# Kernel optimization log

Hardware: AMD Instinct MI355X
Metric: run time of the kernel (lower is better)

Reference implementation:

```python
import jax, jax.numpy as jnp
import numpy as np

SINKHORN_ITERS = 20
EPS = 1e-6


def sinkhorn(M, n_iter=SINKHORN_ITERS, eps=EPS):
    # Project (n, n) logits onto the Birkhoff polytope (doubly stochastic).
    A = jnp.exp(M - jnp.max(M, axis=(-2, -1), keepdims=True))
    for _ in range(n_iter):
        A = A / (A.sum(axis=-1, keepdims=True) + eps)
        A = A / (A.sum(axis=-2, keepdims=True) + eps)
    return A


def setup_inputs() -> dict:
    key = jax.random.key(0)
    k1, k2, k3, k4 = jax.random.split(key, 4)
    B, S, D, E = 4, 4096, 4096, 4
    return {
        "x": jax.random.normal(k1, (B, S, D), dtype=jnp.float32),
        "H_res_logits": jax.random.normal(k2, (E, E), dtype=jnp.float32),
        "H_pre_logits": jax.random.normal(k3, (E, D), dtype=jnp.float32),
        "H_post_logits": jax.random.normal(k4, (E, D), dtype=jnp.float32),
    }


def reference(x, H_res_logits, H_pre_logits, H_post_logits):
    # MHCLayer forward with layer=None (residual routing only), sinkhorn projection.
    H_res = sinkhorn(H_res_logits)                      # (E, E) doubly stochastic
    H_pre = jax.nn.softmax(H_pre_logits, axis=-1)       # (E, D)
    H_post = jax.nn.softmax(H_post_logits, axis=-1)     # (E, D)

    # x_pre = (x.unsqueeze(-2) * H_pre).sum(-1)  ==  x @ H_pre^T
    x_pre = jnp.einsum("bsd,ed->bse", x, H_pre)         # (B, S, E)
    out_exp = x_pre @ H_res                             # (B, S, E)
    # out = (out_exp.unsqueeze(-1) * H_post).sum(-2)  ==  out_exp @ H_post
    out = jnp.einsum("bse,ed->bsd", out_exp, H_post)    # (B, S, D)
    return out
```

## Files before the change

kernel.cpp:

```cpp
#include <hip/hip_runtime.h>
#include <math.h>

#define E 4
#define TPB 256
#define RPB 8
#define NWAVES (TPB / 64)
#define SINKHORN_ITERS 20
#define SINKHORN_EPS 1e-6f

typedef float f4 __attribute__((ext_vector_type(4)));


__global__ __launch_bounds__(TPB) void prep_stats(
    const float* __restrict__ Hres_l,
    const float* __restrict__ Hpre_l,
    const float* __restrict__ Hpost_l,
    float* __restrict__ ws_small,
    int D4)
{
    const int t = threadIdx.x;
    const int wave = t >> 6;
    const int lane = t & 63;

    if (blockIdx.x == 8) {
        if (wave == 0) {
            float a = (lane < E * E) ? Hres_l[lane] : -1e30f;
            float m = a;
#pragma unroll
            for (int off = 1; off < 16; off <<= 1)
                m = fmaxf(m, __shfl_xor(m, off, 16));
            a = expf(a - m);
            for (int it = 0; it < SINKHORN_ITERS; ++it) {
                float rs = a;
                rs += __shfl_xor(rs, 1, 4);
                rs += __shfl_xor(rs, 2, 4);
                a /= (rs + SINKHORN_EPS);
                float cs = a;
                cs += __shfl_xor(cs, 4, 16);
                cs += __shfl_xor(cs, 8, 16);
                a /= (cs + SINKHORN_EPS);
            }
            if (lane < E * E) ws_small[lane] = a;
        }
        return;
    }

    __shared__ float redm[NWAVES], reds[NWAVES];
    const int p = blockIdx.x;
    const int mat = p >> 2, e = p & 3;
    const f4* rowp = (const f4*)((mat ? Hpost_l : Hpre_l) + (size_t)e * D4 * 4);

    float m = -1e30f;
    for (int i = t; i < D4; i += TPB) {
        f4 v = rowp[i];
        m = fmaxf(fmaxf(fmaxf(m, v.x), v.y), fmaxf(v.z, v.w));
    }
#pragma unroll
    for (int off = 1; off < 64; off <<= 1)
        m = fmaxf(m, __shfl_xor(m, off, 64));
    if (lane == 0) redm[wave] = m;
    __syncthreads();
    m = fmaxf(fmaxf(redm[0], redm[1]), fmaxf(redm[2], redm[3]));

    float s = 0.f;
    for (int i = t; i < D4; i += TPB) {
        f4 v = rowp[i];
        s += expf(v.x - m) + expf(v.y - m) + expf(v.z - m) + expf(v.w - m);
    }
#pragma unroll
    for (int off = 1; off < 64; off <<= 1)
        s += __shfl_xor(s, off, 64);
    if (lane == 0) reds[wave] = s;
    __syncthreads();
    if (t == 0) {
        ws_small[16 + p] = m;
        ws_small[24 + p] = reds[0] + reds[1] + reds[2] + reds[3];
    }
}

__global__ __launch_bounds__(TPB) void prep_write(
    const float* __restrict__ Hpre_l,
    const float* __restrict__ Hpost_l,
    const float* __restrict__ ws_small,
    f4* __restrict__ wpre4,
    f4* __restrict__ wpost4,
    int D4)
{
    const int i = blockIdx.x * TPB + threadIdx.x;
    if (i >= D4) return;

    float hres[E * E];
#pragma unroll
    for (int k = 0; k < E * E; ++k) hres[k] = ws_small[k];
    float mpre[E], spre[E], mpost[E], spost[E];
#pragma unroll
    for (int e = 0; e < E; ++e) {
        mpre[e]  = ws_small[16 + e];     spre[e]  = 1.f / ws_small[24 + e];
        mpost[e] = ws_small[16 + E + e]; spost[e] = 1.f / ws_small[24 + E + e];
    }

    const f4* pre_l4  = (const f4*)Hpre_l;
    const f4* post_l4 = (const f4*)Hpost_l;
    f4 postv[E];
#pragma unroll
    for (int e = 0; e < E; ++e) {
        f4 v = pre_l4[(size_t)e * D4 + i];
        f4 o;
        o.x = expf(v.x - mpre[e]) * spre[e];
        o.y = expf(v.y - mpre[e]) * spre[e];
        o.z = expf(v.z - mpre[e]) * spre[e];
        o.w = expf(v.w - mpre[e]) * spre[e];
        wpre4[(size_t)e * D4 + i] = o;
        f4 w = post_l4[(size_t)e * D4 + i];
        postv[e].x = expf(w.x - mpost[e]) * spost[e];
        postv[e].y = expf(w.y - mpost[e]) * spost[e];
        postv[e].z = expf(w.z - mpost[e]) * spost[e];
        postv[e].w = expf(w.w - mpost[e]) * spost[e];
    }
#pragma unroll
    for (int ep = 0; ep < E; ++ep) {
        f4 o = hres[ep * E + 0] * postv[0] + hres[ep * E + 1] * postv[1] +
               hres[ep * E + 2] * postv[2] + hres[ep * E + 3] * postv[3];
        wpost4[(size_t)ep * D4 + i] = o;
    }
}

__global__ __launch_bounds__(TPB) void xpre_kernel(
    const f4* __restrict__ x4,
    const f4* __restrict__ pre4,
    float* __restrict__ xpre,
    int D4, int chunks)
{
    __shared__ float wred[NWAVES][RPB * E];
    const int t = threadIdx.x;
    const int wave = t >> 6;
    const int lane = t & 63;
    const long row0 = (long)blockIdx.x * RPB;

    float val[RPB * E];
#pragma unroll
    for (int i = 0; i < RPB * E; ++i) val[i] = 0.f;

    for (int k = 0; k < chunks; ++k) {
        const int d4 = k * TPB + t;
        f4 hp[E];
#pragma unroll
        for (int e = 0; e < E; ++e) hp[e] = pre4[(size_t)e * D4 + d4];
#pragma unroll
        for (int r = 0; r < RPB; ++r) {
            f4 xv = __builtin_nontemporal_load(&x4[(row0 + r) * D4 + d4]);
#pragma unroll
            for (int e = 0; e < E; ++e)
                val[r * E + e] += xv.x * hp[e].x + xv.y * hp[e].y +
                                  xv.z * hp[e].z + xv.w * hp[e].w;
        }
    }

    {
        const bool h0 = lane & 1;
        float a16[16];
#pragma unroll
        for (int i = 0; i < 16; ++i) {
            float send = h0 ? val[2 * i] : val[2 * i + 1];
            float recv = __shfl_xor(send, 1, 64);
            a16[i] = (h0 ? val[2 * i + 1] : val[2 * i]) + recv;
        }
        const bool h1 = (lane >> 1) & 1;
        float a8[8];
#pragma unroll
        for (int i = 0; i < 8; ++i) {
            float send = h1 ? a16[2 * i] : a16[2 * i + 1];
            float recv = __shfl_xor(send, 2, 64);
            a8[i] = (h1 ? a16[2 * i + 1] : a16[2 * i]) + recv;
        }
        const bool h2 = (lane >> 2) & 1;
        float a4[4];
#pragma unroll
        for (int i = 0; i < 4; ++i) {
            float send = h2 ? a8[2 * i] : a8[2 * i + 1];
            float recv = __shfl_xor(send, 4, 64);
            a4[i] = (h2 ? a8[2 * i + 1] : a8[2 * i]) + recv;
        }
        const bool h3 = (lane >> 3) & 1;
        float a2[2];
#pragma unroll
        for (int i = 0; i < 2; ++i) {
            float send = h3 ? a4[2 * i] : a4[2 * i + 1];
            float recv = __shfl_xor(send, 8, 64);
            a2[i] = (h3 ? a4[2 * i + 1] : a4[2 * i]) + recv;
        }
        const bool h4 = (lane >> 4) & 1;
        float send = h4 ? a2[0] : a2[1];
        float recv = __shfl_xor(send, 16, 64);
        float a1 = (h4 ? a2[1] : a2[0]) + recv;
        a1 += __shfl_xor(a1, 32, 64);
        if (lane < 32) wred[wave][lane] = a1;
    }
    __syncthreads();

    if (t < RPB * E) {
        float s = wred[0][t] + wred[1][t] + wred[2][t] + wred[3][t];
        const int r = t >> 2, e = t & 3;
        xpre[(row0 + r) * E + e] = s;
    }
}

__global__ __launch_bounds__(TPB) void out_kernel(
    const float* __restrict__ xpre,
    const f4* __restrict__ post4,
    f4* __restrict__ out4,
    int D4, int chunks)
{
    __shared__ float sxp[RPB * E];
    const int t = threadIdx.x;
    const long row0 = (long)blockIdx.x * RPB;

    if (t < RPB * E) sxp[t] = xpre[row0 * E + t];
    __syncthreads();

    float xp[RPB][E];
#pragma unroll
    for (int r = 0; r < RPB; ++r)
#pragma unroll
        for (int e = 0; e < E; ++e) xp[r][e] = sxp[r * E + e];

    for (int k = 0; k < chunks; ++k) {
        const int d4 = k * TPB + t;
        f4 hq[E];
#pragma unroll
        for (int e = 0; e < E; ++e) hq[e] = post4[(size_t)e * D4 + d4];
#pragma unroll
        for (int r = 0; r < RPB; ++r) {
            f4 o = xp[r][0] * hq[0] + xp[r][1] * hq[1] +
                   xp[r][2] * hq[2] + xp[r][3] * hq[3];
            __builtin_nontemporal_store(o, &out4[(row0 + r) * D4 + d4]);
        }
    }
}

extern "C" void kernel_launch(void* const* d_in, const int* in_sizes, int n_in,
                              void* d_out, int out_size, void* d_ws, size_t ws_size,
                              hipStream_t stream) {
    const float* x     = (const float*)d_in[0];
    const float* Hres  = (const float*)d_in[1];
    const float* Hpre  = (const float*)d_in[2];
    const float* Hpost = (const float*)d_in[3];
    float* out = (float*)d_out;

    const int D = in_sizes[2] / E;
    const long rows = (long)in_sizes[0] / D;
    const int D4 = D / 4;
    const int chunks = D4 / TPB;

    float* ws_pre   = (float*)d_ws;
    float* ws_post2 = ws_pre + (size_t)E * D;
    float* ws_small = ws_post2 + (size_t)E * D;
    float* ws_xpre  = ws_small + 32;

    prep_stats<<<9, TPB, 0, stream>>>(Hres, Hpre, Hpost, ws_small, D4);
    prep_write<<<(D4 + TPB - 1) / TPB, TPB, 0, stream>>>(
        Hpre, Hpost, ws_small, (f4*)ws_pre, (f4*)ws_post2, D4);

    const int grid = (int)(rows / RPB);
    xpre_kernel<<<grid, TPB, 0, stream>>>((const f4*)x, (const f4*)ws_pre,
                                          ws_xpre, D4, chunks);
    out_kernel<<<grid, TPB, 0, stream>>>(ws_xpre, (const f4*)ws_post2,
                                         (f4*)out, D4, chunks);
}
```

Baseline: 111.0 us.

## Merge softmax prep kernels and fold Sinkhorn into output kernel

Combines the two softmax preparation kernels into one kernel per row that computes max, sum and the normalized write, removing one launch. The Sinkhorn projection moves into every out_kernel block, and H_res is applied to the per-row x_pre values instead of being premultiplied into H_post. This removes a small-kernel launch and dependency from the critical path. In exchange, each output block repeats the 20-iteration Sinkhorn computation redundantly, and the prep kernel now runs on only 8 blocks doing three passes.

```diff
diff --git a/kernel.cpp b/kernel.cpp
--- a/kernel.cpp
+++ b/kernel.cpp
@@ -11,44 +11,21 @@
 typedef float f4 __attribute__((ext_vector_type(4)));
 
 
-__global__ __launch_bounds__(TPB) void prep_stats(
-    const float* __restrict__ Hres_l,
+__global__ __launch_bounds__(TPB) void prep(
     const float* __restrict__ Hpre_l,
     const float* __restrict__ Hpost_l,
-    float* __restrict__ ws_small,
+    f4* __restrict__ wpre4,
+    f4* __restrict__ wpost4,
     int D4)
 {
+    __shared__ float redm[NWAVES], reds[NWAVES];
     const int t = threadIdx.x;
     const int wave = t >> 6;
     const int lane = t & 63;
-
-    if (blockIdx.x == 8) {
-        if (wave == 0) {
-            float a = (lane < E * E) ? Hres_l[lane] : -1e30f;
-            float m = a;
-#pragma unroll
-            for (int off = 1; off < 16; off <<= 1)
-                m = fmaxf(m, __shfl_xor(m, off, 16));
-            a = expf(a - m);
-            for (int it = 0; it < SINKHORN_ITERS; ++it) {
-                float rs = a;
-                rs += __shfl_xor(rs, 1, 4);
-                rs += __shfl_xor(rs, 2, 4);
-                a /= (rs + SINKHORN_EPS);
-                float cs = a;
-                cs += __shfl_xor(cs, 4, 16);
-                cs += __shfl_xor(cs, 8, 16);
-                a /= (cs + SINKHORN_EPS);
-            }
-            if (lane < E * E) ws_small[lane] = a;
-        }
-        return;
-    }
-
-    __shared__ float redm[NWAVES], reds[NWAVES];
     const int p = blockIdx.x;
     const int mat = p >> 2, e = p & 3;
     const f4* rowp = (const f4*)((mat ? Hpost_l : Hpre_l) + (size_t)e * D4 * 4);
+    f4* dst = (mat ? wpost4 : wpre4) + (size_t)e * D4;
 
     float m = -1e30f;
     for (int i = t; i < D4; i += TPB) {
@@ -72,56 +49,16 @@
         s += __shfl_xor(s, off, 64);
     if (lane == 0) reds[wave] = s;
     __syncthreads();
-    if (t == 0) {
-        ws_small[16 + p] = m;
-        ws_small[24 + p] = reds[0] + reds[1] + reds[2] + reds[3];
-    }
-}
-
-__global__ __launch_bounds__(TPB) void prep_write(
-    const float* __restrict__ Hpre_l,
-    const float* __restrict__ Hpost_l,
-    const float* __restrict__ ws_small,
-    f4* __restrict__ wpre4,
-    f4* __restrict__ wpost4,
-    int D4)
-{
-    const int i = blockIdx.x * TPB + threadIdx.x;
-    if (i >= D4) return;
-
-    float hres[E * E];
-#pragma unroll
-    for (int k = 0; k < E * E; ++k) hres[k] = ws_small[k];
-    float mpre[E], spre[E], mpost[E], spost[E];
-#pragma unroll
-    for (int e = 0; e < E; ++e) {
-        mpre[e]  = ws_small[16 + e];     spre[e]  = 1.f / ws_small[24 + e];
-        mpost[e] = ws_small[16 + E + e]; spost[e] = 1.f / ws_small[24 + E + e];
-    }
-
-    const f4* pre_l4  = (const f4*)Hpre_l;
-    const f4* post_l4 = (const f4*)Hpost_l;
-    f4 postv[E];
-#pragma unroll
-    for (int e = 0; e < E; ++e) {
-        f4 v = pre_l4[(size_t)e * D4 + i];
+    const float inv = 1.f / (reds[0] + reds[1] + reds[2] + reds[3]);
+
+    for (int i = t; i < D4; i += TPB) {
+        f4 v = rowp[i];
         f4 o;
-        o.x = expf(v.x - mpre[e]) * spre[e];
-        o.y = expf(v.y - mpre[e]) * spre[e];
-        o.z = expf(v.z - mpre[e]) * spre[e];
-        o.w = expf(v.w - mpre[e]) * spre[e];
-        wpre4[(size_t)e * D4 + i] = o;
-        f4 w = post_l4[(size_t)e * D4 + i];
-        postv[e].x = expf(w.x - mpost[e]) * spost[e];
-        postv[e].y = expf(w.y - mpost[e]) * spost[e];
-        postv[e].z = expf(w.z - mpost[e]) * spost[e];
-        postv[e].w = expf(w.w - mpost[e]) * spost[e];
-    }
-#pragma unroll
-    for (int ep = 0; ep < E; ++ep) {
-        f4 o = hres[ep * E + 0] * postv[0] + hres[ep * E + 1] * postv[1] +
-               hres[ep * E + 2] * postv[2] + hres[ep * E + 3] * postv[3];
-        wpost4[(size_t)ep * D4 + i] = o;
+        o.x = expf(v.x - m) * inv;
+        o.y = expf(v.y - m) * inv;
+        o.z = expf(v.z - m) * inv;
+        o.w = expf(v.w - m) * inv;
+        dst[i] = o;
     }
 }
 
@@ -208,21 +145,48 @@
 __global__ __launch_bounds__(TPB) void out_kernel(
     const float* __restrict__ xpre,
     const f4* __restrict__ post4,
+    const float* __restrict__ HresL,
     f4* __restrict__ out4,
     int D4, int chunks)
 {
+    __shared__ float sHres[E * E];
     __shared__ float sxp[RPB * E];
     const int t = threadIdx.x;
+    const int wave = t >> 6;
+    const int lane = t & 63;
     const long row0 = (long)blockIdx.x * RPB;
 
-    if (t < RPB * E) sxp[t] = xpre[row0 * E + t];
-    __syncthreads();
-
-    float xp[RPB][E];
+    if (wave == 0) {
+        float a = (lane < E * E) ? HresL[lane] : -1e30f;
+        float m = a;
+#pragma unroll
+        for (int off = 1; off < 16; off <<= 1)
+            m = fmaxf(m, __shfl_xor(m, off, 16));
+        a = expf(a - m);
+        for (int it = 0; it < SINKHORN_ITERS; ++it) {
+            float rs = a;
+            rs += __shfl_xor(rs, 1, 4);
+            rs += __shfl_xor(rs, 2, 4);
+            a /= (rs + SINKHORN_EPS);
+            float cs = a;
+            cs += __shfl_xor(cs, 4, 16);
+            cs += __shfl_xor(cs, 8, 16);
+            a /= (cs + SINKHORN_EPS);
+        }
+        if (lane < E * E) sHres[lane] = a;
+    }
+    if (t >= 64 && t < 64 + RPB * E) sxp[t - 64] = xpre[row0 * E + (t - 64)];
+    __syncthreads();
+
+    float xp2[RPB][E];
 #pragma unroll
     for (int r = 0; r < RPB; ++r)
 #pragma unroll
-        for (int e = 0; e < E; ++e) xp[r][e] = sxp[r * E + e];
+        for (int e = 0; e < E; ++e)
+            xp2[r][e] = sxp[r * E + 0] * sHres[0 * E + e] +
+                        sxp[r * E + 1] * sHres[1 * E + e] +
+                        sxp[r * E + 2] * sHres[2 * E + e] +
+                        sxp[r * E + 3] * sHres[3 * E + e];
 
     for (int k = 0; k < chunks; ++k) {
         const int d4 = k * TPB + t;
@@ -231,8 +195,8 @@
         for (int e = 0; e < E; ++e) hq[e] = post4[(size_t)e * D4 + d4];
 #pragma unroll
         for (int r = 0; r < RPB; ++r) {
-            f4 o = xp[r][0] * hq[0] + xp[r][1] * hq[1] +
-                   xp[r][2] * hq[2] + xp[r][3] * hq[3];
+            f4 o = xp2[r][0] * hq[0] + xp2[r][1] * hq[1] +
+                   xp2[r][2] * hq[2] + xp2[r][3] * hq[3];
             __builtin_nontemporal_store(o, &out4[(row0 + r) * D4 + d4]);
         }
     }
@@ -252,18 +216,16 @@
     const int D4 = D / 4;
     const int chunks = D4 / TPB;
 
-    float* ws_pre   = (float*)d_ws;
-    float* ws_post2 = ws_pre + (size_t)E * D;
-    float* ws_small = ws_post2 + (size_t)E * D;
-    float* ws_xpre  = ws_small + 32;
-
-    prep_stats<<<9, TPB, 0, stream>>>(Hres, Hpre, Hpost, ws_small, D4);
-    prep_write<<<(D4 + TPB - 1) / TPB, TPB, 0, stream>>>(
-        Hpre, Hpost, ws_small, (f4*)ws_pre, (f4*)ws_post2, D4);
+    float* ws_pre     = (float*)d_ws;
+    float* ws_post_sm = ws_pre + (size_t)E * D;
+    float* ws_xpre    = ws_post_sm + (size_t)E * D;
+
+    prep<<<2 * E, TPB, 0, stream>>>(Hpre, Hpost, (f4*)ws_pre,
+                                    (f4*)ws_post_sm, D4);
 
     const int grid = (int)(rows / RPB);
     xpre_kernel<<<grid, TPB, 0, stream>>>((const f4*)x, (const f4*)ws_pre,
                                           ws_xpre, D4, chunks);
-    out_kernel<<<grid, TPB, 0, stream>>>(ws_xpre, (const f4*)ws_post2,
-                                         (f4*)out, D4, chunks);
-}
+    out_kernel<<<grid, TPB, 0, stream>>>(ws_xpre, (const f4*)ws_post_sm,
+                                         Hres, (f4*)out, D4, chunks);
+}
```

After: 114.6 us. 1.03x slower.
